# Kernel tuning notes

Measured on AMD Instinct MI355X. Metric: run time of the kernel, lower is better.

The kernel has to match this reference:

```python
import jax, jax.numpy as jnp
import numpy as np

B, S, D_IN, D_OUT = 2, 4096, 512, 512


def setup_inputs() -> dict:
    key = jax.random.key(0)
    k1, k2, k3, k4 = jax.random.split(key, 4)
    x = jax.random.normal(k1, (B, S, D_IN), dtype=jnp.float32)
    # weights stored as [d_in, d_out] so projection is x @ W
    W_query = jax.random.normal(k2, (D_IN, D_OUT), dtype=jnp.float32) * (D_IN ** -0.5)
    W_key = jax.random.normal(k3, (D_IN, D_OUT), dtype=jnp.float32) * (D_IN ** -0.5)
    W_value = jax.random.normal(k4, (D_IN, D_OUT), dtype=jnp.float32) * (D_IN ** -0.5)
    return {"x": x, "W_query": W_query, "W_key": W_key, "W_value": W_value}


def reference(x, W_query, W_key, W_value):
    # Faithful to source: masked_fill is called non-in-place and its result
    # discarded, so NO causal mask is actually applied. Dropout prob = 0.0.
    d_out = W_query.shape[-1]
    q = jnp.einsum('bsi,io->bso', x, W_query)  # [B,S,D_OUT]
    k = jnp.einsum('bsi,io->bso', x, W_key)
    v = jnp.einsum('bsi,io->bso', x, W_value)
    scores = jnp.einsum('bqd,bkd->bqk', q, k) / jnp.sqrt(jnp.float32(d_out))
    weights = jax.nn.softmax(scores, axis=-1)  # [B,S,S]
    context = jnp.einsum('bqk,bkd->bqd', weights, v)  # [B,S,D_OUT]
    return context
```

## Files before the change

kernel.cpp:

```cpp
#include <hip/hip_runtime.h>
#include <cstdint>
#include <cstddef>

typedef unsigned short u16;
typedef __attribute__((ext_vector_type(8))) short bf16x8;
typedef __attribute__((ext_vector_type(4))) float f32x4;

struct alignas(8) u16x4_t { u16 x, y, z, w; };

__device__ __forceinline__ u16 f2bf(float f) {
  uint32_t u = __builtin_bit_cast(uint32_t, f);
  u += 0x7FFFu + ((u >> 16) & 1u);
  return (u16)(u >> 16);
}
__device__ __forceinline__ float bf2f(u16 h) {
  uint32_t u = ((uint32_t)h) << 16;
  return __builtin_bit_cast(float, u);
}

__device__ __forceinline__ void g2l16(const u16* g, u16* l) {
  __builtin_amdgcn_global_load_lds(
      (const __attribute__((address_space(1))) void*)g,
      (__attribute__((address_space(3))) void*)l, 16, 0, 0);
}

#define S_WAITCNT_VM(N) \
  __builtin_amdgcn_s_waitcnt((((N) & 0xF)) | (0x7 << 4) | (0xF << 8) | ((((N) >> 4) & 3) << 14))
#define S_WAITCNT_LGKM0 __builtin_amdgcn_s_waitcnt(0xC07F)

template <int DEPTH, int BM, int BN>
__device__ __forceinline__ void gemm_bt_pipe(
    const u16* __restrict__ A, const u16* __restrict__ Bt,
    int lda, int ldb, int kIters, int m0, int n0,
    u16* sh, f32x4 (&acc)[BM / 32][BN / 32]) {
  constexpr int MI = BM / 32;
  constexpr int NI = BN / 32;
  constexpr int T = (BM + BN) / 64;
  constexpr int SLOT = (BM + BN) * 32;
  constexpr int WVM = T * (DEPTH - 1);
  const int tid = threadIdx.x;
  const int lane = tid & 63, wave = tid >> 6;
  const int wm = wave >> 1, wn = wave & 1, lr = lane & 15, quad = lane >> 4;

  const u16* gp[T];
#pragma unroll
  for (int t = 0; t < T; ++t) {
    const int c = t * 256 + wave * 64 + lane;
    if (c < BM * 4) {
      const int r = c >> 2;
      const int s = (c & 3) ^ ((r >> 1) & 3);
      gp[t] = A + (size_t)(m0 + r) * lda + s * 8;
    } else {
      const int cb = c - BM * 4;
      const int r = cb >> 2;
      const int s = (cb & 3) ^ ((r >> 1) & 3);
      gp[t] = Bt + (size_t)(n0 + r) * ldb + s * 8;
    }
  }
  const int wo = wave * 512;

  auto issue = [&](int slot, int kb) {
    u16* s = sh + slot * SLOT;
#pragma unroll
    for (int t = 0; t < T; ++t)
      g2l16(gp[t] + kb, s + t * 2048 + wo);
  };

#pragma unroll
  for (int p = 0; p < DEPTH; ++p)
    issue(p, (p < kIters ? p : kIters - 1) * 32);

  const int xq = (quad ^ ((lr >> 1) & 3)) * 8;
  for (int kt = 0; kt < kIters; ++kt) {
    S_WAITCNT_VM(WVM);
    __builtin_amdgcn_s_barrier();
    u16* slot = sh + (kt % DEPTH) * SLOT;
    u16* sB = slot + BM * 32;
    bf16x8 af[MI], bfr[NI];
#pragma unroll
    for (int mi = 0; mi < MI; ++mi)
      af[mi] = *(const bf16x8*)(slot + ((wm * (BM / 2) + mi * 16 + lr) * 32 + xq));
#pragma unroll
    for (int ni = 0; ni < NI; ++ni)
      bfr[ni] = *(const bf16x8*)(sB + ((wn * (BN / 2) + ni * 16 + lr) * 32 + xq));
    S_WAITCNT_LGKM0;
    __builtin_amdgcn_s_barrier();
    const int kn = kt + DEPTH;
    issue(kn % DEPTH, (kn < kIters ? kn : kIters - 1) * 32);
#pragma unroll
    for (int mi = 0; mi < MI; ++mi)
#pragma unroll
      for (int ni = 0; ni < NI; ++ni)
        acc[mi][ni] = __builtin_amdgcn_mfma_f32_16x16x32_bf16(af[mi], bfr[ni], acc[mi][ni], 0, 0, 0);
  }
}

#define ZERO_ACC4(acc)                        \
  _Pragma("unroll") for (int mi = 0; mi < 4; ++mi) \
  _Pragma("unroll") for (int ni = 0; ni < 4; ++ni) \
      acc[mi][ni] = f32x4{0.f, 0.f, 0.f, 0.f};

__device__ __forceinline__ void epilogue_ct16(
    const f32x4 (&acc)[4][4], u16* __restrict__ base, int m0w, int n0w,
    int ld, int lane, bool do_exp, float scale, float* rs) {
  const int lr = lane & 15, quad = lane >> 4;
  const int j = quad >> 1, par = quad & 1;
#pragma unroll
  for (int mp = 0; mp < 2; ++mp) {
#pragma unroll
    for (int ni = 0; ni < 4; ++ni) {
      uint32_t p0[2], p1[2];
#pragma unroll
      for (int h = 0; h < 2; ++h) {
        const f32x4 v = acc[mp * 2 + h][ni];
        float e0, e1, e2, e3;
        if (do_exp) {
          e0 = __expf(v[0] * scale); e1 = __expf(v[1] * scale);
          e2 = __expf(v[2] * scale); e3 = __expf(v[3] * scale);
        } else {
          e0 = v[0]; e1 = v[1]; e2 = v[2]; e3 = v[3];
        }
        const u16 h0 = f2bf(e0), h1 = f2bf(e1), h2 = f2bf(e2), h3 = f2bf(e3);
        p0[h] = (uint32_t)h0 | ((uint32_t)h1 << 16);
        p1[h] = (uint32_t)h2 | ((uint32_t)h3 << 16);
        if (rs) rs[ni] += bf2f(h0) + bf2f(h1) + bf2f(h2) + bf2f(h3);
      }
      const uint32_t s0 = par ? p0[0] : p0[1];
      const uint32_t s1 = par ? p1[0] : p1[1];
      const uint32_t r0 = (uint32_t)__shfl_xor((int)s0, 16);
      const uint32_t r1 = (uint32_t)__shfl_xor((int)s1, 16);
      uint4 st;
      if (!par) { st.x = p0[0]; st.y = p1[0]; st.z = r0;    st.w = r1;    }
      else      { st.x = r0;    st.y = r1;    st.z = p0[1]; st.w = p1[1]; }
      const int m = m0w + 16 * (mp * 2 + par) + 8 * j;
      const int n = n0w + ni * 16 + lr;
      *(uint4*)(base + (size_t)n * ld + m) = st;
    }
  }
}

__global__ __launch_bounds__(256) void prep_kernel(
    const float* __restrict__ x, u16* __restrict__ Xb,
    const float* __restrict__ W0, const float* __restrict__ W1,
    const float* __restrict__ W2, u16* __restrict__ Wt,
    float* __restrict__ L) {
  __shared__ float tile[32][33];
  const int id = blockIdx.x;
  if (id < 4096) {
    const int i = (id * 256 + threadIdx.x) * 4;
    const float4 v = *(const float4*)(x + i);
    u16x4_t h;
    h.x = f2bf(v.x); h.y = f2bf(v.y); h.z = f2bf(v.z); h.w = f2bf(v.w);
    *(u16x4_t*)(Xb + i) = h;
    return;
  }
  if (id >= 4864) {
    L[(id - 4864) * 256 + threadIdx.x] = 0.f;
    return;
  }
  const int t = id - 4096;
  const int wz = t >> 8, rem = t & 255;
  const float* W = wz == 0 ? W0 : (wz == 1 ? W1 : W2);
  u16* out = Wt + (size_t)wz * 512 * 512;
  const int bx = (rem & 15) * 32;
  const int by = (rem >> 4) * 32;
  const int tx = threadIdx.x & 31, ty = threadIdx.x >> 5;
#pragma unroll
  for (int i = 0; i < 32; i += 8)
    tile[ty + i][tx] = W[(size_t)(by + ty + i) * 512 + bx + tx];
  __syncthreads();
#pragma unroll
  for (int i = 0; i < 32; i += 8)
    out[(size_t)(bx + ty + i) * 512 + by + tx] = f2bf(tile[tx][ty + i]);
}

__global__ __launch_bounds__(256) void qkv_kernel(
    const u16* __restrict__ Xb, const u16* __restrict__ Wt,
    u16* __restrict__ Qb, u16* __restrict__ Kb, u16* __restrict__ Vt) {
  __shared__ u16 sh[2 * 8192];
  const int z = blockIdx.z;
  int m0, n0;
  const u16 *A, *Bt;
  if (z < 2) {
    m0 = blockIdx.y * 128;
    n0 = blockIdx.x * 128;
    A = Wt + (size_t)z * 512 * 512;
    Bt = Xb;
  } else {
    m0 = blockIdx.x * 128;
    n0 = blockIdx.y * 128;
    A = Xb;
    Bt = Wt + (size_t)2 * 512 * 512;
  }
  f32x4 acc[4][4];
  ZERO_ACC4(acc);
  gemm_bt_pipe<2, 128, 128>(A, Bt, 512, 512, 16, m0, n0, sh, acc);

  const int lane = threadIdx.x & 63, wave = threadIdx.x >> 6;
  const int wm = wave >> 1, wn = wave & 1;
  if (z < 2) {
    epilogue_ct16(acc, z == 0 ? Qb : Kb, m0 + wm * 64, n0 + wn * 64, 512,
                  lane, false, 1.f, nullptr);
  } else {
    const int bb = m0 >> 12;
    epilogue_ct16(acc, Vt + (size_t)bb * 512 * 4096,
                  (m0 & 4095) + wm * 64, n0 + wn * 64, 4096,
                  lane, false, 1.f, nullptr);
  }
}

__global__ __launch_bounds__(256) void scores_kernel(
    const u16* __restrict__ Qb, const u16* __restrict__ Kb,
    u16* __restrict__ P, float* __restrict__ L) {
  __shared__ u16 sh[2 * 8192];
  const int id = blockIdx.x;
  const int qx = (id & 7) * 4 + ((id >> 3) & 3);
  const int ky = (id >> 5) & 31;
  const int b  = id >> 10;
  const int m0 = ky * 128;
  const int n0 = qx * 128;
  f32x4 acc[4][4];
  ZERO_ACC4(acc);
  gemm_bt_pipe<2, 128, 128>(Kb + (size_t)b * 4096 * 512, Qb + (size_t)b * 4096 * 512,
                            512, 512, 16, m0, n0, sh, acc);

  const int lane = threadIdx.x & 63, wave = threadIdx.x >> 6;
  const int wm = wave >> 1, wn = wave & 1, lr = lane & 15, quad = lane >> 4;
  const float scale = 0.04419417382415922f;
  u16* Pb = P + (size_t)b * 4096 * 4096;

  float rs[4] = {0.f, 0.f, 0.f, 0.f};
  epilogue_ct16(acc, Pb, m0 + wm * 64, n0 + wn * 64, 4096, lane, true, scale, rs);

#pragma unroll
  for (int ni = 0; ni < 4; ++ni) {
    float v = rs[ni];
    v += __shfl_xor(v, 16);
    v += __shfl_xor(v, 32);
    if (quad == 0)
      atomicAdd(&L[b * 4096 + n0 + wn * 64 + ni * 16 + lr], v);
  }
}

__global__ __launch_bounds__(256) void pv_kernel(
    const u16* __restrict__ P, const u16* __restrict__ Vt,
    float* __restrict__ part0, float* __restrict__ out) {
  __shared__ u16 sh[3 * 8192];
  const int b = blockIdx.z;
  const int id = blockIdx.x;
  const int ntile = (id >> 3) & 3;
  const int rest = (id & 7) | ((id >> 5) << 3);
  const int mtile = rest & 31;
  const int ks = rest >> 5;
  const int m0 = mtile * 128;
  const int n0 = ntile * 128;
  const int k0 = ks * 2048;
  f32x4 acc[4][4];
  ZERO_ACC4(acc);
  gemm_bt_pipe<3, 128, 128>(P + (size_t)b * 4096 * 4096 + k0,
                            Vt + (size_t)b * 512 * 4096 + k0,
                            4096, 4096, 64, m0, n0, sh, acc);

  const int lane = threadIdx.x & 63, wave = threadIdx.x >> 6;
  const int wm = wave >> 1, wn = wave & 1, lr = lane & 15, quad = lane >> 4;
  float* dst = ks ? out : part0;
#pragma unroll
  for (int mi = 0; mi < 4; ++mi) {
    const int row = m0 + wm * 64 + mi * 16 + quad * 4;
#pragma unroll
    for (int ni = 0; ni < 4; ++ni) {
      const int col = n0 + wn * 64 + ni * 16 + lr;
#pragma unroll
      for (int i = 0; i < 4; ++i)
        dst[(size_t)b * 2097152 + (size_t)(row + i) * 512 + col] = acc[mi][ni][i];
    }
  }
}

__global__ __launch_bounds__(256) void reduce_kernel(
    const float* __restrict__ part0, const float* __restrict__ L,
    float* __restrict__ out) {
  const int i = (blockIdx.x * 256 + threadIdx.x) * 4;
  const float rinv = 1.0f / L[i >> 9];
  const float4 a = *(const float4*)(out + i);
  const float4 p = *(const float4*)(part0 + i);
  float4 r;
  r.x = (a.x + p.x) * rinv; r.y = (a.y + p.y) * rinv;
  r.z = (a.z + p.z) * rinv; r.w = (a.w + p.w) * rinv;
  *(float4*)(out + i) = r;
}

extern "C" void kernel_launch(void* const* d_in, const int* in_sizes, int n_in,
                              void* d_out, int out_size, void* d_ws, size_t ws_size,
                              hipStream_t stream) {
  const float* x  = (const float*)d_in[0];
  const float* Wq = (const float*)d_in[1];
  const float* Wk = (const float*)d_in[2];
  const float* Wv = (const float*)d_in[3];
  float* out = (float*)d_out;
  char* ws = (char*)d_ws;
  u16* Xb = (u16*)(ws);
  u16* Qb = (u16*)(ws + 8388608);
  u16* Kb = (u16*)(ws + 16777216);
  u16* Vt = (u16*)(ws + 25165824);
  u16* Wt = (u16*)(ws + 33554432);
  u16* P  = (u16*)(ws + 35127296);
  float* L = (float*)(ws + 102236160);
  float* part0 = (float*)(ws + 8388608);

  prep_kernel<<<4896, 256, 0, stream>>>(x, Xb, Wq, Wk, Wv, Wt, L);
  qkv_kernel<<<dim3(64, 4, 3), 256, 0, stream>>>(Xb, Wt, Qb, Kb, Vt);
  scores_kernel<<<2048, 256, 0, stream>>>(Qb, Kb, P, L);
  pv_kernel<<<dim3(256, 1, 2), 256, 0, stream>>>(P, Vt, part0, out);
  reduce_kernel<<<4096, 256, 0, stream>>>(part0, L, out);
}
```

Before: 197.6 us.

## Enlarge scores GEMM tile to 256x256 with 8 waves and 3-stage pipeline

The scores kernel moves from 128x128 tiles on 4 waves to 256x256 tiles on 8 waves (512 threads), using a new 3-deep global-to-LDS pipeline with 96KB of dynamic shared memory. Larger tiles cut the global/L2 traffic per MFMA and halve the number of blocks, improving operand reuse for the QK^T product. In exchange, per-thread accumulator registers double and only 512 blocks are launched, which may hurt occupancy and load balance across CUs.

```diff
diff --git a/kernel.cpp b/kernel.cpp
--- a/kernel.cpp
+++ b/kernel.cpp
@@ -95,18 +95,86 @@
   }
 }
 
+template <int DEPTH, int BM, int BN>
+__device__ __forceinline__ void gemm_bt_pipe_w8(
+    const u16* __restrict__ A, const u16* __restrict__ Bt,
+    int lda, int ldb, int kIters, int m0, int n0,
+    u16* sh, f32x4 (&acc)[BM / 32][BN / 64]) {
+  constexpr int MI = BM / 32;
+  constexpr int NI = BN / 64;
+  constexpr int T = (BM + BN) / 128;
+  constexpr int SLOT = (BM + BN) * 32;
+  constexpr int WVM = T * (DEPTH - 1);
+  const int tid = threadIdx.x;
+  const int lane = tid & 63, wave = tid >> 6;
+  const int wm = wave >> 2, wn = wave & 3, lr = lane & 15, quad = lane >> 4;
+
+  const u16* gp[T];
+#pragma unroll
+  for (int t = 0; t < T; ++t) {
+    const int c = t * 512 + wave * 64 + lane;
+    if (c < BM * 4) {
+      const int r = c >> 2;
+      const int s = (c & 3) ^ ((r >> 1) & 3);
+      gp[t] = A + (size_t)(m0 + r) * lda + s * 8;
+    } else {
+      const int cb = c - BM * 4;
+      const int r = cb >> 2;
+      const int s = (cb & 3) ^ ((r >> 1) & 3);
+      gp[t] = Bt + (size_t)(n0 + r) * ldb + s * 8;
+    }
+  }
+  const int wo = wave * 512;
+
+  auto issue = [&](int slot, int kb) {
+    u16* s = sh + slot * SLOT;
+#pragma unroll
+    for (int t = 0; t < T; ++t)
+      g2l16(gp[t] + kb, s + t * 4096 + wo);
+  };
+
+#pragma unroll
+  for (int p = 0; p < DEPTH; ++p)
+    issue(p, (p < kIters ? p : kIters - 1) * 32);
+
+  const int xq = (quad ^ ((lr >> 1) & 3)) * 8;
+  for (int kt = 0; kt < kIters; ++kt) {
+    S_WAITCNT_VM(WVM);
+    __builtin_amdgcn_s_barrier();
+    u16* slot = sh + (kt % DEPTH) * SLOT;
+    u16* sB = slot + BM * 32;
+    bf16x8 af[MI], bfr[NI];
+#pragma unroll
+    for (int mi = 0; mi < MI; ++mi)
+      af[mi] = *(const bf16x8*)(slot + ((wm * (BM / 2) + mi * 16 + lr) * 32 + xq));
+#pragma unroll
+    for (int ni = 0; ni < NI; ++ni)
+      bfr[ni] = *(const bf16x8*)(sB + ((wn * (BN / 4) + ni * 16 + lr) * 32 + xq));
+    S_WAITCNT_LGKM0;
+    __builtin_amdgcn_s_barrier();
+    const int kn = kt + DEPTH;
+    issue(kn % DEPTH, (kn < kIters ? kn : kIters - 1) * 32);
+#pragma unroll
+    for (int mi = 0; mi < MI; ++mi)
+#pragma unroll
+      for (int ni = 0; ni < NI; ++ni)
+        acc[mi][ni] = __builtin_amdgcn_mfma_f32_16x16x32_bf16(af[mi], bfr[ni], acc[mi][ni], 0, 0, 0);
+  }
+}
+
 #define ZERO_ACC4(acc)                        \
   _Pragma("unroll") for (int mi = 0; mi < 4; ++mi) \
   _Pragma("unroll") for (int ni = 0; ni < 4; ++ni) \
       acc[mi][ni] = f32x4{0.f, 0.f, 0.f, 0.f};
 
+template <int MI>
 __device__ __forceinline__ void epilogue_ct16(
-    const f32x4 (&acc)[4][4], u16* __restrict__ base, int m0w, int n0w,
+    const f32x4 (&acc)[MI][4], u16* __restrict__ base, int m0w, int n0w,
     int ld, int lane, bool do_exp, float scale, float* rs) {
   const int lr = lane & 15, quad = lane >> 4;
   const int j = quad >> 1, par = quad & 1;
 #pragma unroll
-  for (int mp = 0; mp < 2; ++mp) {
+  for (int mp = 0; mp < MI / 2; ++mp) {
 #pragma unroll
     for (int ni = 0; ni < 4; ++ni) {
       uint32_t p0[2], p1[2];
@@ -199,38 +267,46 @@
   const int lane = threadIdx.x & 63, wave = threadIdx.x >> 6;
   const int wm = wave >> 1, wn = wave & 1;
   if (z < 2) {
-    epilogue_ct16(acc, z == 0 ? Qb : Kb, m0 + wm * 64, n0 + wn * 64, 512,
-                  lane, false, 1.f, nullptr);
+    epilogue_ct16<4>(acc, z == 0 ? Qb : Kb, m0 + wm * 64, n0 + wn * 64, 512,
+                     lane, false, 1.f, nullptr);
   } else {
     const int bb = m0 >> 12;
-    epilogue_ct16(acc, Vt + (size_t)bb * 512 * 4096,
-                  (m0 & 4095) + wm * 64, n0 + wn * 64, 4096,
-                  lane, false, 1.f, nullptr);
-  }
-}
-
-__global__ __launch_bounds__(256) void scores_kernel(
+    epilogue_ct16<4>(acc, Vt + (size_t)bb * 512 * 4096,
+                     (m0 & 4095) + wm * 64, n0 + wn * 64, 4096,
+                     lane, false, 1.f, nullptr);
+  }
+}
+
+__global__ __launch_bounds__(512, 2) void scores_kernel(
     const u16* __restrict__ Qb, const u16* __restrict__ Kb,
     u16* __restrict__ P, float* __restrict__ L) {
-  __shared__ u16 sh[2 * 8192];
+  extern __shared__ u16 sh[];
   const int id = blockIdx.x;
-  const int qx = (id & 7) * 4 + ((id >> 3) & 3);
-  const int ky = (id >> 5) & 31;
-  const int b  = id >> 10;
-  const int m0 = ky * 128;
-  const int n0 = qx * 128;
-  f32x4 acc[4][4];
-  ZERO_ACC4(acc);
-  gemm_bt_pipe<2, 128, 128>(Kb + (size_t)b * 4096 * 512, Qb + (size_t)b * 4096 * 512,
-                            512, 512, 16, m0, n0, sh, acc);
+  const int b = id >> 8;
+  const int r = id & 255;
+  const int j = r >> 3;
+  const int qx = (r & 7) * 2 + (j >> 4);
+  const int ky = j & 15;
+  const int m0 = ky * 256;
+  const int n0 = qx * 256;
+  f32x4 acc[8][4];
+#pragma unroll
+  for (int mi = 0; mi < 8; ++mi)
+#pragma unroll
+    for (int ni = 0; ni < 4; ++ni)
+      acc[mi][ni] = f32x4{0.f, 0.f, 0.f, 0.f};
+  gemm_bt_pipe_w8<3, 256, 256>(Kb + (size_t)b * 4096 * 512,
+                               Qb + (size_t)b * 4096 * 512,
+                               512, 512, 16, m0, n0, sh, acc);
 
   const int lane = threadIdx.x & 63, wave = threadIdx.x >> 6;
-  const int wm = wave >> 1, wn = wave & 1, lr = lane & 15, quad = lane >> 4;
+  const int wm = wave >> 2, wn = wave & 3, lr = lane & 15, quad = lane >> 4;
   const float scale = 0.04419417382415922f;
   u16* Pb = P + (size_t)b * 4096 * 4096;
 
   float rs[4] = {0.f, 0.f, 0.f, 0.f};
-  epilogue_ct16(acc, Pb, m0 + wm * 64, n0 + wn * 64, 4096, lane, true, scale, rs);
+  epilogue_ct16<8>(acc, Pb, m0 + wm * 128, n0 + wn * 64, 4096, lane, true,
+                   scale, rs);
 
 #pragma unroll
   for (int ni = 0; ni < 4; ++ni) {
@@ -308,9 +384,16 @@
   float* L = (float*)(ws + 102236160);
   float* part0 = (float*)(ws + 8388608);
 
+  static bool attr_set = false;
+  if (!attr_set) {
+    hipFuncSetAttribute(reinterpret_cast<const void*>(scores_kernel),
+                        hipFuncAttributeMaxDynamicSharedMemorySize, 98304);
+    attr_set = true;
+  }
+
   prep_kernel<<<4896, 256, 0, stream>>>(x, Xb, Wq, Wk, Wv, Wt, L);
   qkv_kernel<<<dim3(64, 4, 3), 256, 0, stream>>>(Xb, Wt, Qb, Kb, Vt);
-  scores_kernel<<<2048, 256, 0, stream>>>(Qb, Kb, P, L);
+  scores_kernel<<<512, 512, 98304, stream>>>(Qb, Kb, P, L);
   pv_kernel<<<dim3(256, 1, 2), 256, 0, stream>>>(P, Vt, part0, out);
   reduce_kernel<<<4096, 256, 0, stream>>>(part0, L, out);
 }
```

Result: no change. 197.0 us (-0.3%).
